# Kernel tuning notes

Hardware: AMD Instinct MI355X
Metric: run time of the kernel (lower is better)

## Reference

```python
import jax, jax.numpy as jnp
import numpy as np

D = 512      # d_model
H = 8        # heads
DK = D // H  # 64
DFF = 2048
EPS = 1e-6


def layer_norm(x, gamma, beta):
    # Faithful to the module: std uses Bessel correction (torch default unbiased)
    # and eps is added to std (not variance); gamma/beta are scalars init to 1.
    m = jnp.mean(x, axis=-1, keepdims=True)
    var = jnp.sum((x - m) ** 2, axis=-1, keepdims=True) / (x.shape[-1] - 1)
    return gamma * (x - m) / (jnp.sqrt(var) + EPS) + beta


def setup_inputs() -> dict:
    key = jax.random.key(0)
    ks = jax.random.split(key, 12)
    s = 0.02
    inp = {
        "x": jax.random.normal(ks[0], (4, 2048, D), dtype=jnp.float32),
        "src_mask": jnp.ones((4, 1, 1, 2048), dtype=jnp.int32),
        "Wq": jax.random.normal(ks[1], (D, D), jnp.float32) * s,
        "bq": jnp.zeros((D,), jnp.float32),
        "Wk": jax.random.normal(ks[2], (D, D), jnp.float32) * s,
        "bk": jnp.zeros((D,), jnp.float32),
        "Wv": jax.random.normal(ks[3], (D, D), jnp.float32) * s,
        "bv": jnp.zeros((D,), jnp.float32),
        "Wo": jax.random.normal(ks[4], (D, D), jnp.float32) * s,
        "bo": jnp.zeros((D,), jnp.float32),
        "W1": jax.random.normal(ks[5], (D, DFF), jnp.float32) * s,
        "b1": jnp.zeros((DFF,), jnp.float32),
        "W2": jax.random.normal(ks[6], (DFF, D), jnp.float32) * s,
        "b2": jnp.zeros((D,), jnp.float32),
        "g1": jnp.ones((), jnp.float32),
        "be1": jnp.ones((), jnp.float32),
        "g2": jnp.ones((), jnp.float32),
        "be2": jnp.ones((), jnp.float32),
    }
    return inp


def reference(x, src_mask, Wq, bq, Wk, bk, Wv, bv, Wo, bo,
              W1, b1, W2, b2, g1, be1, g2, be2):
    B, S, _ = x.shape

    # --- residual 1: pre-LN self-attention ---
    xn = layer_norm(x, g1, be1)                               # [B,S,D]
    q = (xn @ Wq + bq).reshape(B, S, H, DK).transpose(0, 2, 1, 3)  # [B,H,S,DK]
    k = (xn @ Wk + bk).reshape(B, S, H, DK).transpose(0, 2, 1, 3)
    v = (xn @ Wv + bv).reshape(B, S, H, DK).transpose(0, 2, 1, 3)

    scores = jnp.einsum('bhqd,bhkd->bhqk', q, k) / np.float32(np.sqrt(DK))
    scores = jnp.where(src_mask == 0, jnp.float32(-1e9), scores)  # [B,H,S,S]
    attn = jax.nn.softmax(scores, axis=-1)
    o = jnp.einsum('bhqk,bhkd->bhqd', attn, v)                # [B,H,S,DK]
    o = o.transpose(0, 2, 1, 3).reshape(B, S, D)
    x = x + (o @ Wo + bo)

    # --- residual 2: pre-LN feed-forward ---
    xn = layer_norm(x, g2, be2)
    ff = jax.nn.relu(xn @ W1 + b1) @ W2 + b2
    return x + ff
```

## Files before the change

### kernel.cpp

```cpp
#include <hip/hip_runtime.h>
#include <hip/hip_bf16.h>


#define B_   4
#define S_   2048
#define D_   512
#define H_   8
#define DK_  64
#define DFF_ 2048
#define M_   (B_*S_)

typedef __attribute__((ext_vector_type(8))) short short8;
typedef __attribute__((ext_vector_type(4))) float f32x4;
typedef __attribute__((ext_vector_type(16))) float f32x16;

#define QSCALE 0.18033688011f

#if __has_builtin(__builtin_amdgcn_exp2f)
#define EXP2(x) __builtin_amdgcn_exp2f(x)
#else
#define EXP2(x) exp2f(x)
#endif

#define GLOAD_LDS(gp, lp) __builtin_amdgcn_global_load_lds( \
    (const __attribute__((address_space(1))) void*)(gp),    \
    (__attribute__((address_space(3))) void*)(lp), 16, 0, 0)

#define WAITV(N) asm volatile("s_waitcnt vmcnt(" #N ")" ::: "memory")
#define BARRIER() __builtin_amdgcn_s_barrier()

__device__ inline unsigned short f2bf(float f) {
    union { float f; unsigned u; } v; v.f = f;
    unsigned r = v.u + 0x7fffu + ((v.u >> 16) & 1u);
    return (unsigned short)(r >> 16);
}

__device__ inline unsigned cvtpk_bf16(float a, float b) {
    unsigned r;
    asm("v_cvt_pk_bf16_f32 %0, %1, %2" : "=v"(r) : "v"(a), "v"(b));
    return r;
}

__device__ inline void permswap32(unsigned &x, unsigned &y) {
    asm volatile("v_permlane32_swap_b32 %0, %1" : "+v"(x), "+v"(y));
}

__global__ __launch_bounds__(256) void transT_kernel(
    const float* __restrict__ Wq, const float* __restrict__ Wk,
    const float* __restrict__ Wv, const float* __restrict__ Wo,
    const float* __restrict__ W1, const float* __restrict__ W2,
    const float* __restrict__ bq, const float* __restrict__ bk,
    const float* __restrict__ bv, const int* __restrict__ mask,
    float* __restrict__ qkvb, unsigned* __restrict__ mbits,
    short* __restrict__ dst,
    const float* __restrict__ x, const float* __restrict__ g1,
    const float* __restrict__ be1, short* __restrict__ xn) {
    const int id = blockIdx.x, t = threadIdx.x;
    if (id >= 769) {
        int w = t >> 6, l = t & 63;
        int row = (id - 769) * 4 + w;
        const float4* xr = (const float4*)(x + (size_t)row * D_);
        float4 a = xr[l * 2], b = xr[l * 2 + 1];
        float s = a.x + a.y + a.z + a.w + b.x + b.y + b.z + b.w;
        for (int off = 32; off > 0; off >>= 1) s += __shfl_xor(s, off);
        float mean = s * (1.f / 512.f);
        float e[8] = {a.x - mean, a.y - mean, a.z - mean, a.w - mean,
                      b.x - mean, b.y - mean, b.z - mean, b.w - mean};
        float vs = 0.f;
        #pragma unroll
        for (int i = 0; i < 8; i++) vs += e[i] * e[i];
        for (int off = 32; off > 0; off >>= 1) vs += __shfl_xor(vs, off);
        float scale = g1[0] / (sqrtf(vs * (1.f / 511.f)) + 1e-6f);
        float b0 = be1[0];
        union { short8 v; short s[8]; } o;
        #pragma unroll
        for (int i = 0; i < 8; i++) o.s[i] = (short)f2bf(e[i] * scale + b0);
        *(short8*)(xn + (size_t)row * D_ + l * 8) = o.v;
        return;
    }
    if (id == 768) {
        for (int i = t; i < 1536; i += 256)
            qkvb[i] = (i < 512) ? bq[i] * QSCALE : (i < 1024) ? bk[i - 512] : bv[i - 1024];
        if (t < 128) {
            int b = t >> 5, tile = t & 31;
            const int* mr = mask + b * S_ + tile * 64;
            bool all1 = true;
            for (int u = 0; u < 64; u++) all1 &= (mr[u] != 0);
            unsigned long long bal = __ballot(all1);
            if ((t & 63) == 0) {
                mbits[(t >> 6) * 2]     = (unsigned)bal;
                mbits[(t >> 6) * 2 + 1] = (unsigned)(bal >> 32);
            }
        }
        return;
    }
    __shared__ float T[64][65];
    const float* src; short* d; int K, N, tk, tn;
    if (id < 256) {
        int m = id >> 6;
        src = (m == 0) ? Wq : (m == 1) ? Wk : (m == 2) ? Wv : Wo;
        d = dst + (size_t)m * 512 * 512; K = 512; N = 512;
        int j = id & 63; tk = j >> 3; tn = j & 7;
    } else if (id < 512) {
        src = W1; d = dst + (size_t)4 * 512 * 512; K = 512; N = 2048;
        int j = id - 256; tk = j >> 5; tn = j & 31;
    } else {
        src = W2; d = dst + (size_t)4 * 512 * 512 + 2048 * 512; K = 2048; N = 512;
        int j = id - 512; tk = j >> 3; tn = j & 7;
    }
    const int k0 = tk * 64, n0 = tn * 64;
    #pragma unroll
    for (int i = 0; i < 4; i++) {
        int r = i * 16 + (t >> 4), c4 = (t & 15) * 4;
        float4 v = *(const float4*)(src + (size_t)(k0 + r) * N + n0 + c4);
        T[r][c4] = v.x; T[r][c4 + 1] = v.y; T[r][c4 + 2] = v.z; T[r][c4 + 3] = v.w;
    }
    __syncthreads();
    #pragma unroll
    for (int p = 0; p < 2; p++) {
        int j = p * 256 + t, n = j >> 3, kc = (j & 7) * 8;
        union { short8 v; short s[8]; } o;
        #pragma unroll
        for (int u = 0; u < 8; u++) o.s[u] = (short)f2bf(T[kc + u][n]);
        *(short8*)(d + (size_t)(n0 + n) * K + k0 + kc) = o.v;
    }
}

__global__ __launch_bounds__(256) void ln_kernel(const float* __restrict__ x,
                                                 const float* __restrict__ g,
                                                 const float* __restrict__ be,
                                                 short* __restrict__ out) {
    int w = threadIdx.x >> 6, l = threadIdx.x & 63;
    int row = blockIdx.x * 4 + w;
    const float4* xr = (const float4*)(x + (size_t)row * D_);
    float4 a = xr[l * 2], b = xr[l * 2 + 1];
    float s = a.x + a.y + a.z + a.w + b.x + b.y + b.z + b.w;
    for (int off = 32; off > 0; off >>= 1) s += __shfl_xor(s, off);
    float mean = s * (1.f / 512.f);
    float e[8] = {a.x - mean, a.y - mean, a.z - mean, a.w - mean,
                  b.x - mean, b.y - mean, b.z - mean, b.w - mean};
    float vs = 0.f;
    #pragma unroll
    for (int i = 0; i < 8; i++) vs += e[i] * e[i];
    for (int off = 32; off > 0; off >>= 1) vs += __shfl_xor(vs, off);
    float scale = g[0] / (sqrtf(vs * (1.f / 511.f)) + 1e-6f);
    float b0 = be[0];
    union { short8 v; short s[8]; } o;
    #pragma unroll
    for (int i = 0; i < 8; i++) o.s[i] = (short)f2bf(e[i] * scale + b0);
    *(short8*)(out + (size_t)row * D_ + l * 8) = o.v;
}

template <int BN, int MODE>
__global__ __launch_bounds__(256, 4) void gemm_kernel(
    const short* __restrict__ A, const short* __restrict__ Bt,
    const float* __restrict__ bias, const float* __restrict__ resid,
    void* __restrict__ out, int M, int N, int K) {
    constexpr int NF = BN / 32;
    __shared__ __align__(16) short smem[3 * 128 * 32 + 3 * BN * 32];
    auto As = [&](int b) -> short* { return smem + b * 4096; };
    auto Bs = [&](int b) -> short* { return smem + 12288 + b * BN * 32; };
    const int t = threadIdx.x;
    const int w = t >> 6, l = t & 63;
    const int wm = w >> 1, wn = w & 1;
    const int lr = l & 15, lk = l >> 4;
    const int m0 = blockIdx.x * 128, n0 = blockIdx.y * BN;
    f32x4 acc[4][NF] = {};

    auto stage = [&](int buf, int k0) {
        #pragma unroll
        for (int p = 0; p < 2; p++) {
            int g = p * 4 + w;
            int r = g * 16 + (l >> 2), c = l & 3, cs = c ^ ((r >> 2) & 3);
            GLOAD_LDS(A + (size_t)(m0 + r) * K + k0 + cs * 8, As(buf) + g * 512);
        }
        #pragma unroll
        for (int p = 0; p < BN / 64; p++) {
            int g = p * 4 + w;
            int r = g * 16 + (l >> 2), c = l & 3, cs = c ^ ((r >> 2) & 3);
            GLOAD_LDS(Bt + (size_t)(n0 + r) * K + k0 + cs * 8, Bs(buf) + g * 512);
        }
    };

    const int nk = K >> 5;
    stage(0, 0); stage(1, 32);
    if constexpr (BN == 128) WAITV(4); else WAITV(3);
    BARRIER();

    for (int tk = 0; tk < nk; ++tk) {
        const int cur = tk % 3;
        const bool more = (tk + 2 < nk);
        if (more) stage((tk + 2) % 3, (tk + 2) * 32);
        short8 af[4], bf[NF];
        #pragma unroll
        for (int f = 0; f < 4; f++) {
            int ra = wm * 64 + f * 16 + lr;
            af[f] = *(const short8*)&As(cur)[ra * 32 + ((lk ^ ((ra >> 2) & 3)) << 3)];
        }
        #pragma unroll
        for (int f = 0; f < NF; f++) {
            int rb = wn * (BN / 2) + f * 16 + lr;
            bf[f] = *(const short8*)&Bs(cur)[rb * 32 + ((lk ^ ((rb >> 2) & 3)) << 3)];
        }
        __builtin_amdgcn_s_setprio(1);
        #pragma unroll
        for (int mf = 0; mf < 4; mf++)
            #pragma unroll
            for (int nf = 0; nf < NF; nf++)
                acc[mf][nf] = __builtin_amdgcn_mfma_f32_16x16x32_bf16(
                    af[mf], bf[nf], acc[mf][nf], 0, 0, 0);
        __builtin_amdgcn_s_setprio(0);
        if (more) { if constexpr (BN == 128) WAITV(4); else WAITV(3); }
        else WAITV(0);
        BARRIER();
    }

    if constexpr (MODE == 0) {
        const int seg = n0 >> 9;
        #pragma unroll
        for (int mf = 0; mf < 4; mf++) {
            #pragma unroll
            for (int nf = 0; nf < NF; nf++) {
                int mb = m0 + wm * 64 + mf * 16 + lk * 4;
                int n  = n0 + wn * (BN / 2) + nf * 16 + lr;
                float bv = bias[n];
                int bb = mb >> 11, sl = mb & 2047, nl = n & 511;
                unsigned short* ob = (unsigned short*)out + (size_t)seg * M_ * D_;
                float v[4];
                #pragma unroll
                for (int i = 0; i < 4; i++) {
                    float val = acc[mf][nf][i];
                    if (seg == 0) val *= QSCALE;
                    v[i] = val + bv;
                }
                if (seg < 2) {
                    #pragma unroll
                    for (int i = 0; i < 4; i++)
                        ob[(((size_t)(bb * 8 + (nl >> 6)) * 2048 + sl + i) << 6) + (nl & 63)] = f2bf(v[i]);
                } else {
                    uint2 pk;
                    pk.x = cvtpk_bf16(v[0], v[1]);
                    pk.y = cvtpk_bf16(v[2], v[3]);
                    *(uint2*)&ob[(((size_t)(bb * 8 + (nl >> 6)) * 64 + (nl & 63)) << 11) + sl] = pk;
                }
            }
        }
    } else if constexpr (MODE == 1) {
        float* E = (float*)smem;
        #pragma unroll
        for (int mf = 0; mf < 4; mf++)
            #pragma unroll
            for (int nf = 0; nf < NF; nf++) {
                int n_loc = wn * (BN / 2) + nf * 16 + lr;
                float bv = bias[n0 + n_loc];
                int c = n_loc >> 4;
                #pragma unroll
                for (int i = 0; i < 4; i++) {
                    int m_loc = wm * 64 + mf * 16 + lk * 4 + i;
                    E[m_loc * 64 + ((c ^ (m_loc & 3)) << 4) + (n_loc & 15)] =
                        acc[mf][nf][i] + bv;
                }
            }
        BARRIER();
        #pragma unroll
        for (int pass = 0; pass < 8; pass++) {
            int fid = pass * 256 + t;
            int row = fid >> 4, c4 = fid & 15;
            int lc = c4 >> 2, j = c4 & 3;
            f32x4 v = *(f32x4*)&E[row * 64 + (((lc ^ (row & 3))) << 4) + j * 4];
            int m = m0 + row, n = n0 + lc * 16 + j * 4;
            f32x4 rv = *(const f32x4*)&resid[(size_t)m * N + n];
            *(f32x4*)&((float*)out)[(size_t)m * N + n] = v + rv;
        }
    } else {
        unsigned short* E16 = (unsigned short*)smem;
        #pragma unroll
        for (int mf = 0; mf < 4; mf++)
            #pragma unroll
            for (int nf = 0; nf < NF; nf++) {
                int n_loc = wn * (BN / 2) + nf * 16 + lr;
                float bv = bias[n0 + n_loc];
                int c = n_loc >> 3;
                #pragma unroll
                for (int i = 0; i < 4; i++) {
                    int m_loc = wm * 64 + mf * 16 + lk * 4 + i;
                    E16[m_loc * 128 + ((c ^ (m_loc & 7)) << 3) + (n_loc & 7)] =
                        f2bf(fmaxf(acc[mf][nf][i] + bv, 0.f));
                }
            }
        BARRIER();
        #pragma unroll
        for (int pass = 0; pass < 8; pass++) {
            int fid = pass * 256 + t;
            int row = fid >> 4, c = fid & 15;
            short8 v = *(short8*)&E16[row * 128 + ((c ^ (row & 7)) << 3)];
            *(short8*)&((unsigned short*)out)[(size_t)(m0 + row) * N + n0 + c * 8] = v;
        }
    }
}

__global__ __launch_bounds__(512, 4) void attn_kernel(
    const short* __restrict__ Q, const short* __restrict__ Kb,
    const short* __restrict__ Vt, const int* __restrict__ mask,
    const unsigned* __restrict__ mbits, unsigned short* __restrict__ O) {
    __shared__ __align__(16) short sm[24576];
    const int t = threadIdx.x, w = t >> 6, l = t & 63;
    const int ql = l & 31, hi = l >> 5;
    const int wh = w >> 2, wl = w & 3;
    const int bh = blockIdx.x, b = bh >> 3, h = bh & 7;
    const int q = blockIdx.y * 128 + wl * 32 + ql;

    const short* qrow = Q + ((size_t)bh * S_ + q) * DK_;
    short8 qf[4];
    #pragma unroll
    for (int s = 0; s < 4; s++) qf[s] = *(const short8*)(qrow + s * 16 + hi * 8);

    const short* kg = Kb + (size_t)bh * S_ * DK_;
    const short* vg = Vt + (size_t)bh * DK_ * S_;
    const int* mrow = mask + b * S_;
    const unsigned mb = mbits[b];

    short* KH = sm + wh * 12288;
    short* kdw = KH + wl * 512;

    const int kro = wl * 8 + (l >> 3);
    const int kc = (l & 7) ^ (kro & 7);
    const short* kp = kg + ((size_t)(wh * 1024 + kro)) * 64 + kc * 8;
    const int vr = kro, vs0 = l & 7, vc = vs0 ^ (vr & 7);
    const int vdk = vr + 32 * (vc >> 2), vkvo = (vc & 3) * 8;
    const short* vp = vg + (size_t)vdk * 2048 + vkvo + wh * 1024;

    auto stage = [&](int buf) {
        GLOAD_LDS(kp, kdw + buf * 4096);
        GLOAD_LDS(vp, kdw + buf * 4096 + 2048);
        kp += 32 * 64;
        vp += 32;
    };

    const short ONEB = (short)0x3F80;
    const short8 ones = {ONEB, ONEB, ONEB, ONEB, ONEB, ONEB, ONEB, ONEB};

    f32x16 o_acc[2] = {};
    f32x16 lsum = {};

    stage(0); stage(1);
    WAITV(2);
    BARRIER();

    for (int tt = 0; tt < 32; ++tt) {
        const int cur = tt % 3;
        const int gt = wh * 32 + tt;
        if (tt + 2 < 32) stage((tt + 2) % 3);
        const short* Ks = KH + cur * 4096;
        const short* Vs = Ks + 2048;

        f32x16 s_acc = {};
        __builtin_amdgcn_s_setprio(1);
        #pragma unroll
        for (int s = 0; s < 4; s++) {
            short8 kf = *(const short8*)&Ks[ql * 64 + (((s * 2 + hi) ^ (ql & 7)) << 3)];
            s_acc = __builtin_amdgcn_mfma_f32_32x32x16_bf16(kf, qf[s], s_acc, 0, 0, 0);
        }
        __builtin_amdgcn_s_setprio(0);

        if (!((mb >> (gt >> 1)) & 1)) {
            #pragma unroll
            for (int r = 0; r < 16; r++) {
                int k = gt * 32 + (r & 3) + 8 * (r >> 2) + 4 * hi;
                if (mrow[k] == 0) s_acc[r] = -1.4426950e9f;
            }
        }

        float p[16];
        #pragma unroll
        for (int r = 0; r < 16; r++) p[r] = EXP2(s_acc[r]);
        unsigned Dp[8];
        #pragma unroll
        for (int j = 0; j < 8; j++) Dp[j] = cvtpk_bf16(p[2 * j], p[2 * j + 1]);

        #pragma unroll
        for (int s16 = 0; s16 < 2; s16++) {
            unsigned f0 = Dp[s16 * 4 + 0], f1 = Dp[s16 * 4 + 1];
            unsigned f2 = Dp[s16 * 4 + 2], f3 = Dp[s16 * 4 + 3];
            permswap32(f0, f2);
            permswap32(f1, f3);
            union { unsigned u[4]; short8 v; } pu;
            pu.u[0] = f0; pu.u[1] = f1; pu.u[2] = f2; pu.u[3] = f3;
            __builtin_amdgcn_s_setprio(1);
            #pragma unroll
            for (int dt = 0; dt < 2; dt++) {
                short8 vf = *(const short8*)&Vs[ql * 64 + (((dt * 4 + s16 * 2 + hi) ^ (ql & 7)) << 3)];
                o_acc[dt] = __builtin_amdgcn_mfma_f32_32x32x16_bf16(vf, pu.v, o_acc[dt], 0, 0, 0);
            }
            lsum = __builtin_amdgcn_mfma_f32_32x32x16_bf16(ones, pu.v, lsum, 0, 0, 0);
            __builtin_amdgcn_s_setprio(0);
        }

        if (tt < 30) WAITV(2); else WAITV(0);
        BARRIER();
    }

    float l_part = lsum[0];
    float* C = (float*)sm;
    f32x4* Cv = (f32x4*)sm;
    if (wh == 1) {
        #pragma unroll
        for (int j = 0; j < 8; j++) {
            f32x4 v;
            #pragma unroll
            for (int e = 0; e < 4; e++) v[e] = o_acc[j >> 2][(j & 3) * 4 + e];
            Cv[wl * 512 + j * 64 + l] = v;
        }
        C[8192 + wl * 64 + l] = l_part;
    }
    __syncthreads();
    if (wh == 0) {
        #pragma unroll
        for (int j = 0; j < 8; j++) {
            f32x4 v = Cv[wl * 512 + j * 64 + l];
            #pragma unroll
            for (int e = 0; e < 4; e++) o_acc[j >> 2][(j & 3) * 4 + e] += v[e];
        }
        l_part += C[8192 + wl * 64 + l];
        float linv = 1.f / l_part;
        unsigned short* orow = O + ((size_t)b * S_ + q) * D_ + h * 64;
        #pragma unroll
        for (int dt = 0; dt < 2; dt++)
            #pragma unroll
            for (int g = 0; g < 4; g++) {
                unsigned u0 = cvtpk_bf16(o_acc[dt][g * 4 + 0] * linv, o_acc[dt][g * 4 + 1] * linv);
                unsigned u1 = cvtpk_bf16(o_acc[dt][g * 4 + 2] * linv, o_acc[dt][g * 4 + 3] * linv);
                uint2 pk; pk.x = u0; pk.y = u1;
                *(uint2*)(orow + dt * 32 + 8 * g + 4 * hi) = pk;
            }
    }
}

extern "C" void kernel_launch(void* const* d_in, const int* in_sizes, int n_in,
                              void* d_out, int out_size, void* d_ws, size_t ws_size,
                              hipStream_t stream) {
    const float* x    = (const float*)d_in[0];
    const int*   mask = (const int*)d_in[1];
    const float* Wq = (const float*)d_in[2];  const float* bq  = (const float*)d_in[3];
    const float* Wk = (const float*)d_in[4];  const float* bk  = (const float*)d_in[5];
    const float* Wv = (const float*)d_in[6];  const float* bv  = (const float*)d_in[7];
    const float* Wo = (const float*)d_in[8];  const float* bo  = (const float*)d_in[9];
    const float* W1 = (const float*)d_in[10]; const float* b1  = (const float*)d_in[11];
    const float* W2 = (const float*)d_in[12]; const float* b2  = (const float*)d_in[13];
    const float* g1 = (const float*)d_in[14]; const float* be1 = (const float*)d_in[15];
    const float* g2 = (const float*)d_in[16]; const float* be2 = (const float*)d_in[17];

    short* WqT = (short*)d_ws;
    short* W1T = WqT + 4 * 512 * 512;
    short* W2T = W1T + 2048 * 512;
    short* xn  = W2T + 512 * 2048;
    short* Qb  = xn  + (size_t)M_ * D_;
    short* Kbf = Qb  + (size_t)M_ * D_;
    short* Vtb = Kbf + (size_t)M_ * D_;
    short* Ob  = Vtb + (size_t)M_ * D_;
    float* x2  = (float*)(Ob + (size_t)M_ * D_);
    float* qkvb = x2;
    unsigned* mbits = (unsigned*)(qkvb + 1536);
    short* WoT = WqT + 3 * 512 * 512;
    short* Hb  = Qb;

    transT_kernel<<<769 + M_ / 4, 256, 0, stream>>>(Wq, Wk, Wv, Wo, W1, W2,
                                                    bq, bk, bv, mask, qkvb, mbits, WqT,
                                                    x, g1, be1, xn);

    gemm_kernel<128, 0><<<dim3(64, 12), 256, 0, stream>>>(xn, WqT, qkvb, nullptr,
                                                          Qb, M_, 1536, 512);

    attn_kernel<<<dim3(B_ * H_, S_ / 128), 512, 0, stream>>>(Qb, Kbf, Vtb, mask, mbits,
                                                             (unsigned short*)Ob);

    gemm_kernel<64, 1><<<dim3(64, 8), 256, 0, stream>>>(Ob, WoT, bo, x, x2, M_, 512, 512);

    ln_kernel<<<M_ / 4, 256, 0, stream>>>(x2, g2, be2, xn);

    gemm_kernel<128, 2><<<dim3(64, 16), 256, 0, stream>>>(xn, W1T, b1, nullptr, Hb, M_, 2048, 512);
    gemm_kernel<64, 1><<<dim3(64, 8), 256, 0, stream>>>(Hb, W2T, b2, x2, (float*)d_out, M_, 512, 2048);
}
```

Before: 150.7 us.

## Widen GEMM K-tile to 64 with double buffering; attention processes 64 queries per wave

The GEMM now stages 64-wide K slices in two LDS buffers instead of three 32-wide ones, with an 8-way XOR swizzle. This halves the number of barriers and loop iterations but gives up one stage of prefetch depth. The attention kernel now gives each wave two 32-query groups that share the same K/V fragments, halving the grid and reusing K/V loads across more queries. Row sums are accumulated in scalar registers rather than through a ones-matrix MFMA. Register pressure rises, which is reflected in lowering the occupancy hints in launch_bounds to 2.

```diff
diff --git a/kernel.cpp b/kernel.cpp
--- a/kernel.cpp
+++ b/kernel.cpp
@@ -152,14 +152,14 @@
 }
 
 template <int BN, int MODE>
-__global__ __launch_bounds__(256, 4) void gemm_kernel(
+__global__ __launch_bounds__(256, 2) void gemm_kernel(
     const short* __restrict__ A, const short* __restrict__ Bt,
     const float* __restrict__ bias, const float* __restrict__ resid,
     void* __restrict__ out, int M, int N, int K) {
     constexpr int NF = BN / 32;
-    __shared__ __align__(16) short smem[3 * 128 * 32 + 3 * BN * 32];
-    auto As = [&](int b) -> short* { return smem + b * 4096; };
-    auto Bs = [&](int b) -> short* { return smem + 12288 + b * BN * 32; };
+    __shared__ __align__(16) short smem[2 * 128 * 64 + 2 * BN * 64];
+    auto As = [&](int b) -> short* { return smem + b * 8192; };
+    auto Bs = [&](int b) -> short* { return smem + 16384 + b * BN * 64; };
     const int t = threadIdx.x;
     const int w = t >> 6, l = t & 63;
     const int wm = w >> 1, wn = w & 1;
@@ -169,49 +169,54 @@
 
     auto stage = [&](int buf, int k0) {
         #pragma unroll
-        for (int p = 0; p < 2; p++) {
-            int g = p * 4 + w;
-            int r = g * 16 + (l >> 2), c = l & 3, cs = c ^ ((r >> 2) & 3);
-            GLOAD_LDS(A + (size_t)(m0 + r) * K + k0 + cs * 8, As(buf) + g * 512);
-        }
-        #pragma unroll
-        for (int p = 0; p < BN / 64; p++) {
-            int g = p * 4 + w;
-            int r = g * 16 + (l >> 2), c = l & 3, cs = c ^ ((r >> 2) & 3);
-            GLOAD_LDS(Bt + (size_t)(n0 + r) * K + k0 + cs * 8, Bs(buf) + g * 512);
+        for (int p = 0; p < 4; p++) {
+            int id = p * 256 + t;
+            int r = id >> 3, c = id & 7, cs = c ^ (r & 7);
+            GLOAD_LDS(A + (size_t)(m0 + r) * K + k0 + cs * 8, As(buf) + (p * 256 + w * 64) * 8);
+        }
+        #pragma unroll
+        for (int p = 0; p < BN / 32; p++) {
+            int id = p * 256 + t;
+            int r = id >> 3, c = id & 7, cs = c ^ (r & 7);
+            GLOAD_LDS(Bt + (size_t)(n0 + r) * K + k0 + cs * 8, Bs(buf) + (p * 256 + w * 64) * 8);
         }
     };
 
-    const int nk = K >> 5;
-    stage(0, 0); stage(1, 32);
-    if constexpr (BN == 128) WAITV(4); else WAITV(3);
-    BARRIER();
+    const int nk = K >> 6;
+    stage(0, 0);
 
     for (int tk = 0; tk < nk; ++tk) {
-        const int cur = tk % 3;
-        const bool more = (tk + 2 < nk);
-        if (more) stage((tk + 2) % 3, (tk + 2) * 32);
-        short8 af[4], bf[NF];
+        const int cur = tk & 1;
+        if (tk + 1 < nk) {
+            stage(cur ^ 1, (tk + 1) * 64);
+            if constexpr (BN == 128) WAITV(8); else WAITV(6);
+        } else WAITV(0);
+        BARRIER();
+        short8 af[4][2], bf[NF][2];
         #pragma unroll
         for (int f = 0; f < 4; f++) {
             int ra = wm * 64 + f * 16 + lr;
-            af[f] = *(const short8*)&As(cur)[ra * 32 + ((lk ^ ((ra >> 2) & 3)) << 3)];
+            #pragma unroll
+            for (int kk = 0; kk < 2; kk++)
+                af[f][kk] = *(const short8*)&As(cur)[ra * 64 + (((kk * 4 + lk) ^ (ra & 7)) << 3)];
         }
         #pragma unroll
         for (int f = 0; f < NF; f++) {
             int rb = wn * (BN / 2) + f * 16 + lr;
-            bf[f] = *(const short8*)&Bs(cur)[rb * 32 + ((lk ^ ((rb >> 2) & 3)) << 3)];
+            #pragma unroll
+            for (int kk = 0; kk < 2; kk++)
+                bf[f][kk] = *(const short8*)&Bs(cur)[rb * 64 + (((kk * 4 + lk) ^ (rb & 7)) << 3)];
         }
         __builtin_amdgcn_s_setprio(1);
         #pragma unroll
-        for (int mf = 0; mf < 4; mf++)
-            #pragma unroll
-            for (int nf = 0; nf < NF; nf++)
-                acc[mf][nf] = __builtin_amdgcn_mfma_f32_16x16x32_bf16(
-                    af[mf], bf[nf], acc[mf][nf], 0, 0, 0);
+        for (int kk = 0; kk < 2; kk++)
+            #pragma unroll
+            for (int mf = 0; mf < 4; mf++)
+                #pragma unroll
+                for (int nf = 0; nf < NF; nf++)
+                    acc[mf][nf] = __builtin_amdgcn_mfma_f32_16x16x32_bf16(
+                        af[mf][kk], bf[nf][kk], acc[mf][nf], 0, 0, 0);
         __builtin_amdgcn_s_setprio(0);
-        if (more) { if constexpr (BN == 128) WAITV(4); else WAITV(3); }
-        else WAITV(0);
         BARRIER();
     }
 
@@ -299,7 +304,7 @@
     }
 }
 
-__global__ __launch_bounds__(512, 4) void attn_kernel(
+__global__ __launch_bounds__(512, 2) void attn_kernel(
     const short* __restrict__ Q, const short* __restrict__ Kb,
     const short* __restrict__ Vt, const int* __restrict__ mask,
     const unsigned* __restrict__ mbits, unsigned short* __restrict__ O) {
@@ -308,12 +313,15 @@
     const int ql = l & 31, hi = l >> 5;
     const int wh = w >> 2, wl = w & 3;
     const int bh = blockIdx.x, b = bh >> 3, h = bh & 7;
-    const int q = blockIdx.y * 128 + wl * 32 + ql;
-
-    const short* qrow = Q + ((size_t)bh * S_ + q) * DK_;
-    short8 qf[4];
-    #pragma unroll
-    for (int s = 0; s < 4; s++) qf[s] = *(const short8*)(qrow + s * 16 + hi * 8);
+    const int q0 = blockIdx.y * 256 + wl * 64;
+
+    short8 qf[2][4];
+    #pragma unroll
+    for (int qs = 0; qs < 2; qs++) {
+        const short* qrow = Q + ((size_t)bh * S_ + q0 + qs * 32 + ql) * DK_;
+        #pragma unroll
+        for (int s = 0; s < 4; s++) qf[qs][s] = *(const short8*)(qrow + s * 16 + hi * 8);
+    }
 
     const short* kg = Kb + (size_t)bh * S_ * DK_;
     const short* vg = Vt + (size_t)bh * DK_ * S_;
@@ -326,7 +334,7 @@
     const int kro = wl * 8 + (l >> 3);
     const int kc = (l & 7) ^ (kro & 7);
     const short* kp = kg + ((size_t)(wh * 1024 + kro)) * 64 + kc * 8;
-    const int vr = kro, vs0 = l & 7, vc = vs0 ^ (vr & 7);
+    const int vr = kro, vc = (l & 7) ^ (vr & 7);
     const int vdk = vr + 32 * (vc >> 2), vkvo = (vc & 3) * 8;
     const short* vp = vg + (size_t)vdk * 2048 + vkvo + wh * 1024;
 
@@ -337,11 +345,8 @@
         vp += 32;
     };
 
-    const short ONEB = (short)0x3F80;
-    const short8 ones = {ONEB, ONEB, ONEB, ONEB, ONEB, ONEB, ONEB, ONEB};
-
-    f32x16 o_acc[2] = {};
-    f32x16 lsum = {};
+    f32x16 o_acc[2][2] = {};
+    float la[2][4] = {};
 
     stage(0); stage(1);
     WAITV(2);
@@ -354,45 +359,59 @@
         const short* Ks = KH + cur * 4096;
         const short* Vs = Ks + 2048;
 
-        f32x16 s_acc = {};
+        short8 kf[4];
+        #pragma unroll
+        for (int s = 0; s < 4; s++)
+            kf[s] = *(const short8*)&Ks[ql * 64 + (((s * 2 + hi) ^ (ql & 7)) << 3)];
+        f32x16 sa = {}, sb = {};
         __builtin_amdgcn_s_setprio(1);
         #pragma unroll
-        for (int s = 0; s < 4; s++) {
-            short8 kf = *(const short8*)&Ks[ql * 64 + (((s * 2 + hi) ^ (ql & 7)) << 3)];
-            s_acc = __builtin_amdgcn_mfma_f32_32x32x16_bf16(kf, qf[s], s_acc, 0, 0, 0);
-        }
+        for (int s = 0; s < 4; s++)
+            sa = __builtin_amdgcn_mfma_f32_32x32x16_bf16(kf[s], qf[0][s], sa, 0, 0, 0);
+        #pragma unroll
+        for (int s = 0; s < 4; s++)
+            sb = __builtin_amdgcn_mfma_f32_32x32x16_bf16(kf[s], qf[1][s], sb, 0, 0, 0);
         __builtin_amdgcn_s_setprio(0);
 
         if (!((mb >> (gt >> 1)) & 1)) {
             #pragma unroll
             for (int r = 0; r < 16; r++) {
                 int k = gt * 32 + (r & 3) + 8 * (r >> 2) + 4 * hi;
-                if (mrow[k] == 0) s_acc[r] = -1.4426950e9f;
-            }
-        }
-
-        float p[16];
-        #pragma unroll
-        for (int r = 0; r < 16; r++) p[r] = EXP2(s_acc[r]);
-        unsigned Dp[8];
-        #pragma unroll
-        for (int j = 0; j < 8; j++) Dp[j] = cvtpk_bf16(p[2 * j], p[2 * j + 1]);
+                if (mrow[k] == 0) { sa[r] = -1.4426950e9f; sb[r] = -1.4426950e9f; }
+            }
+        }
+
+        unsigned Dp[2][8];
+        {
+            float p[16];
+            #pragma unroll
+            for (int r = 0; r < 16; r++) { p[r] = EXP2(sa[r]); la[0][r & 3] += p[r]; }
+            #pragma unroll
+            for (int j = 0; j < 8; j++) Dp[0][j] = cvtpk_bf16(p[2 * j], p[2 * j + 1]);
+            #pragma unroll
+            for (int r = 0; r < 16; r++) { p[r] = EXP2(sb[r]); la[1][r & 3] += p[r]; }
+            #pragma unroll
+            for (int j = 0; j < 8; j++) Dp[1][j] = cvtpk_bf16(p[2 * j], p[2 * j + 1]);
+        }
 
         #pragma unroll
         for (int s16 = 0; s16 < 2; s16++) {
-            unsigned f0 = Dp[s16 * 4 + 0], f1 = Dp[s16 * 4 + 1];
-            unsigned f2 = Dp[s16 * 4 + 2], f3 = Dp[s16 * 4 + 3];
-            permswap32(f0, f2);
-            permswap32(f1, f3);
-            union { unsigned u[4]; short8 v; } pu;
-            pu.u[0] = f0; pu.u[1] = f1; pu.u[2] = f2; pu.u[3] = f3;
+            union { unsigned u[4]; short8 v; } pu[2];
+            #pragma unroll
+            for (int qs = 0; qs < 2; qs++) {
+                unsigned f0 = Dp[qs][s16 * 4 + 0], f1 = Dp[qs][s16 * 4 + 1];
+                unsigned f2 = Dp[qs][s16 * 4 + 2], f3 = Dp[qs][s16 * 4 + 3];
+                permswap32(f0, f2);
+                permswap32(f1, f3);
+                pu[qs].u[0] = f0; pu[qs].u[1] = f1; pu[qs].u[2] = f2; pu[qs].u[3] = f3;
+            }
             __builtin_amdgcn_s_setprio(1);
             #pragma unroll
             for (int dt = 0; dt < 2; dt++) {
                 short8 vf = *(const short8*)&Vs[ql * 64 + (((dt * 4 + s16 * 2 + hi) ^ (ql & 7)) << 3)];
-                o_acc[dt] = __builtin_amdgcn_mfma_f32_32x32x16_bf16(vf, pu.v, o_acc[dt], 0, 0, 0);
-            }
-            lsum = __builtin_amdgcn_mfma_f32_32x32x16_bf16(ones, pu.v, lsum, 0, 0, 0);
+                o_acc[0][dt] = __builtin_amdgcn_mfma_f32_32x32x16_bf16(vf, pu[0].v, o_acc[0][dt], 0, 0, 0);
+                o_acc[1][dt] = __builtin_amdgcn_mfma_f32_32x32x16_bf16(vf, pu[1].v, o_acc[1][dt], 0, 0, 0);
+            }
             __builtin_amdgcn_s_setprio(0);
         }
 
@@ -400,39 +419,48 @@
         BARRIER();
     }
 
-    float l_part = lsum[0];
+    float lp[2];
+    #pragma unroll
+    for (int qs = 0; qs < 2; qs++) {
+        float s = (la[qs][0] + la[qs][1]) + (la[qs][2] + la[qs][3]);
+        lp[qs] = s + __shfl_xor(s, 32);
+    }
+
     float* C = (float*)sm;
     f32x4* Cv = (f32x4*)sm;
-    if (wh == 1) {
-        #pragma unroll
-        for (int j = 0; j < 8; j++) {
-            f32x4 v;
-            #pragma unroll
-            for (int e = 0; e < 4; e++) v[e] = o_acc[j >> 2][(j & 3) * 4 + e];
-            Cv[wl * 512 + j * 64 + l] = v;
-        }
-        C[8192 + wl * 64 + l] = l_part;
-    }
-    __syncthreads();
-    if (wh == 0) {
-        #pragma unroll
-        for (int j = 0; j < 8; j++) {
-            f32x4 v = Cv[wl * 512 + j * 64 + l];
-            #pragma unroll
-            for (int e = 0; e < 4; e++) o_acc[j >> 2][(j & 3) * 4 + e] += v[e];
-        }
-        l_part += C[8192 + wl * 64 + l];
-        float linv = 1.f / l_part;
-        unsigned short* orow = O + ((size_t)b * S_ + q) * D_ + h * 64;
-        #pragma unroll
-        for (int dt = 0; dt < 2; dt++)
-            #pragma unroll
-            for (int g = 0; g < 4; g++) {
-                unsigned u0 = cvtpk_bf16(o_acc[dt][g * 4 + 0] * linv, o_acc[dt][g * 4 + 1] * linv);
-                unsigned u1 = cvtpk_bf16(o_acc[dt][g * 4 + 2] * linv, o_acc[dt][g * 4 + 3] * linv);
-                uint2 pk; pk.x = u0; pk.y = u1;
-                *(uint2*)(orow + dt * 32 + 8 * g + 4 * hi) = pk;
-            }
+    #pragma unroll
+    for (int qs = 0; qs < 2; qs++) {
+        __syncthreads();
+        if (wh == 1) {
+            #pragma unroll
+            for (int j = 0; j < 8; j++) {
+                f32x4 v;
+                #pragma unroll
+                for (int e = 0; e < 4; e++) v[e] = o_acc[qs][j >> 2][(j & 3) * 4 + e];
+                Cv[wl * 512 + j * 64 + l] = v;
+            }
+            C[8192 + wl * 64 + l] = lp[qs];
+        }
+        __syncthreads();
+        if (wh == 0) {
+            #pragma unroll
+            for (int j = 0; j < 8; j++) {
+                f32x4 v = Cv[wl * 512 + j * 64 + l];
+                #pragma unroll
+                for (int e = 0; e < 4; e++) o_acc[qs][j >> 2][(j & 3) * 4 + e] += v[e];
+            }
+            float linv = 1.f / (lp[qs] + C[8192 + wl * 64 + l]);
+            unsigned short* orow = O + ((size_t)b * S_ + q0 + qs * 32 + ql) * D_ + h * 64;
+            #pragma unroll
+            for (int dt = 0; dt < 2; dt++)
+                #pragma unroll
+                for (int g = 0; g < 4; g++) {
+                    unsigned u0 = cvtpk_bf16(o_acc[qs][dt][g * 4 + 0] * linv, o_acc[qs][dt][g * 4 + 1] * linv);
+                    unsigned u1 = cvtpk_bf16(o_acc[qs][dt][g * 4 + 2] * linv, o_acc[qs][dt][g * 4 + 3] * linv);
+                    uint2 pk; pk.x = u0; pk.y = u1;
+                    *(uint2*)(orow + dt * 32 + 8 * g + 4 * hi) = pk;
+                }
+        }
     }
 }
 
@@ -471,7 +499,7 @@
     gemm_kernel<128, 0><<<dim3(64, 12), 256, 0, stream>>>(xn, WqT, qkvb, nullptr,
                                                           Qb, M_, 1536, 512);
 
-    attn_kernel<<<dim3(B_ * H_, S_ / 128), 512, 0, stream>>>(Qb, Kbf, Vtb, mask, mbits,
+    attn_kernel<<<dim3(B_ * H_, S_ / 256), 512, 0, stream>>>(Qb, Kbf, Vtb, mask, mbits,
                                                              (unsigned short*)Ob);
 
     gemm_kernel<64, 1><<<dim3(64, 8), 256, 0, stream>>>(Ob, WoT, bo, x, x2, M_, 512, 512);
```

Measured after the change: 138.5 us. 1.09x faster.

## Use BK=64 double-buffered GEMM pipeline and scalar softmax row sums in attention

Applied to the files above, without the earlier changes.

The GEMM moves from a triple-buffered K=32 pipeline to a double-buffered K=64 pipeline with an 8-chunk XOR swizzle. This halves the number of barrier/iteration steps and lowers the occupancy hint in launch bounds from 4 to 2. The attention kernel replaces the ones-matrix MFMA used for row sums with VALU accumulation of the exp values plus a cross-half shuffle, freeing matrix-core cycles. The K/V staging is also rewritten to compute addresses from the tile index instead of advancing pointers. The risks are lower occupancy, less latency hiding with only two buffers, and the extra VALU adds.

```diff
diff --git a/kernel.cpp b/kernel.cpp
--- a/kernel.cpp
+++ b/kernel.cpp
@@ -152,14 +152,14 @@
 }
 
 template <int BN, int MODE>
-__global__ __launch_bounds__(256, 4) void gemm_kernel(
+__global__ __launch_bounds__(256, 2) void gemm_kernel(
     const short* __restrict__ A, const short* __restrict__ Bt,
     const float* __restrict__ bias, const float* __restrict__ resid,
     void* __restrict__ out, int M, int N, int K) {
     constexpr int NF = BN / 32;
-    __shared__ __align__(16) short smem[3 * 128 * 32 + 3 * BN * 32];
-    auto As = [&](int b) -> short* { return smem + b * 4096; };
-    auto Bs = [&](int b) -> short* { return smem + 12288 + b * BN * 32; };
+    __shared__ __align__(16) short smem[2 * 128 * 64 + 2 * BN * 64];
+    auto As = [&](int b) -> short* { return smem + b * 8192; };
+    auto Bs = [&](int b) -> short* { return smem + 16384 + b * BN * 64; };
     const int t = threadIdx.x;
     const int w = t >> 6, l = t & 63;
     const int wm = w >> 1, wn = w & 1;
@@ -169,49 +169,54 @@
 
     auto stage = [&](int buf, int k0) {
         #pragma unroll
-        for (int p = 0; p < 2; p++) {
-            int g = p * 4 + w;
-            int r = g * 16 + (l >> 2), c = l & 3, cs = c ^ ((r >> 2) & 3);
-            GLOAD_LDS(A + (size_t)(m0 + r) * K + k0 + cs * 8, As(buf) + g * 512);
-        }
-        #pragma unroll
-        for (int p = 0; p < BN / 64; p++) {
-            int g = p * 4 + w;
-            int r = g * 16 + (l >> 2), c = l & 3, cs = c ^ ((r >> 2) & 3);
-            GLOAD_LDS(Bt + (size_t)(n0 + r) * K + k0 + cs * 8, Bs(buf) + g * 512);
+        for (int p = 0; p < 4; p++) {
+            int id = p * 256 + t;
+            int r = id >> 3, c = id & 7, cs = c ^ (r & 7);
+            GLOAD_LDS(A + (size_t)(m0 + r) * K + k0 + cs * 8, As(buf) + (p * 256 + w * 64) * 8);
+        }
+        #pragma unroll
+        for (int p = 0; p < BN / 32; p++) {
+            int id = p * 256 + t;
+            int r = id >> 3, c = id & 7, cs = c ^ (r & 7);
+            GLOAD_LDS(Bt + (size_t)(n0 + r) * K + k0 + cs * 8, Bs(buf) + (p * 256 + w * 64) * 8);
         }
     };
 
-    const int nk = K >> 5;
-    stage(0, 0); stage(1, 32);
-    if constexpr (BN == 128) WAITV(4); else WAITV(3);
-    BARRIER();
+    const int nk = K >> 6;
+    stage(0, 0);
 
     for (int tk = 0; tk < nk; ++tk) {
-        const int cur = tk % 3;
-        const bool more = (tk + 2 < nk);
-        if (more) stage((tk + 2) % 3, (tk + 2) * 32);
-        short8 af[4], bf[NF];
+        const int cur = tk & 1;
+        if (tk + 1 < nk) {
+            stage(cur ^ 1, (tk + 1) * 64);
+            if constexpr (BN == 128) WAITV(8); else WAITV(6);
+        } else WAITV(0);
+        BARRIER();
+        short8 af[4][2], bf[NF][2];
         #pragma unroll
         for (int f = 0; f < 4; f++) {
             int ra = wm * 64 + f * 16 + lr;
-            af[f] = *(const short8*)&As(cur)[ra * 32 + ((lk ^ ((ra >> 2) & 3)) << 3)];
+            #pragma unroll
+            for (int kk = 0; kk < 2; kk++)
+                af[f][kk] = *(const short8*)&As(cur)[ra * 64 + (((kk * 4 + lk) ^ (ra & 7)) << 3)];
         }
         #pragma unroll
         for (int f = 0; f < NF; f++) {
             int rb = wn * (BN / 2) + f * 16 + lr;
-            bf[f] = *(const short8*)&Bs(cur)[rb * 32 + ((lk ^ ((rb >> 2) & 3)) << 3)];
+            #pragma unroll
+            for (int kk = 0; kk < 2; kk++)
+                bf[f][kk] = *(const short8*)&Bs(cur)[rb * 64 + (((kk * 4 + lk) ^ (rb & 7)) << 3)];
         }
         __builtin_amdgcn_s_setprio(1);
         #pragma unroll
-        for (int mf = 0; mf < 4; mf++)
-            #pragma unroll
-            for (int nf = 0; nf < NF; nf++)
-                acc[mf][nf] = __builtin_amdgcn_mfma_f32_16x16x32_bf16(
-                    af[mf], bf[nf], acc[mf][nf], 0, 0, 0);
+        for (int kk = 0; kk < 2; kk++)
+            #pragma unroll
+            for (int mf = 0; mf < 4; mf++)
+                #pragma unroll
+                for (int nf = 0; nf < NF; nf++)
+                    acc[mf][nf] = __builtin_amdgcn_mfma_f32_16x16x32_bf16(
+                        af[mf][kk], bf[nf][kk], acc[mf][nf], 0, 0, 0);
         __builtin_amdgcn_s_setprio(0);
-        if (more) { if constexpr (BN == 128) WAITV(4); else WAITV(3); }
-        else WAITV(0);
         BARRIER();
     }
 
@@ -321,36 +326,33 @@
     const unsigned mb = mbits[b];
 
     short* KH = sm + wh * 12288;
-    short* kdw = KH + wl * 512;
-
-    const int kro = wl * 8 + (l >> 3);
-    const int kc = (l & 7) ^ (kro & 7);
-    const short* kp = kg + ((size_t)(wh * 1024 + kro)) * 64 + kc * 8;
-    const int vr = kro, vs0 = l & 7, vc = vs0 ^ (vr & 7);
-    const int vdk = vr + 32 * (vc >> 2), vkvo = (vc & 3) * 8;
-    const short* vp = vg + (size_t)vdk * 2048 + vkvo + wh * 1024;
-
-    auto stage = [&](int buf) {
-        GLOAD_LDS(kp, kdw + buf * 4096);
-        GLOAD_LDS(vp, kdw + buf * 4096 + 2048);
-        kp += 32 * 64;
-        vp += 32;
+
+    auto stage = [&](int buf, int kv0) {
+        short* Kd = KH + buf * 4096;
+        short* Vd = Kd + 2048;
+        {
+            int r = wl * 8 + (l >> 3), c = l & 7, cs = c ^ (r & 7);
+            GLOAD_LDS(kg + (size_t)(kv0 + r) * DK_ + cs * 8, &Kd[wl * 512]);
+        }
+        {
+            int r = wl * 8 + (l >> 3), s = l & 7, c = s ^ (r & 7);
+            int dk = r + 32 * (c >> 2), kvo = (c & 3) * 8;
+            GLOAD_LDS(vg + (size_t)dk * S_ + kv0 + kvo, &Vd[wl * 512]);
+        }
     };
 
-    const short ONEB = (short)0x3F80;
-    const short8 ones = {ONEB, ONEB, ONEB, ONEB, ONEB, ONEB, ONEB, ONEB};
-
     f32x16 o_acc[2] = {};
-    f32x16 lsum = {};
-
-    stage(0); stage(1);
+    float la0 = 0.f, la1 = 0.f, la2 = 0.f, la3 = 0.f;
+
+    stage(0, wh * 1024);
+    stage(1, wh * 1024 + 32);
     WAITV(2);
     BARRIER();
 
     for (int tt = 0; tt < 32; ++tt) {
         const int cur = tt % 3;
         const int gt = wh * 32 + tt;
-        if (tt + 2 < 32) stage((tt + 2) % 3);
+        if (tt + 2 < 32) stage((tt + 2) % 3, (gt + 2) * 32);
         const short* Ks = KH + cur * 4096;
         const short* Vs = Ks + 2048;
 
@@ -374,6 +376,10 @@
         float p[16];
         #pragma unroll
         for (int r = 0; r < 16; r++) p[r] = EXP2(s_acc[r]);
+        #pragma unroll
+        for (int r = 0; r < 16; r += 4) {
+            la0 += p[r]; la1 += p[r + 1]; la2 += p[r + 2]; la3 += p[r + 3];
+        }
         unsigned Dp[8];
         #pragma unroll
         for (int j = 0; j < 8; j++) Dp[j] = cvtpk_bf16(p[2 * j], p[2 * j + 1]);
@@ -392,7 +398,6 @@
                 short8 vf = *(const short8*)&Vs[ql * 64 + (((dt * 4 + s16 * 2 + hi) ^ (ql & 7)) << 3)];
                 o_acc[dt] = __builtin_amdgcn_mfma_f32_32x32x16_bf16(vf, pu.v, o_acc[dt], 0, 0, 0);
             }
-            lsum = __builtin_amdgcn_mfma_f32_32x32x16_bf16(ones, pu.v, lsum, 0, 0, 0);
             __builtin_amdgcn_s_setprio(0);
         }
 
@@ -400,7 +405,7 @@
         BARRIER();
     }
 
-    float l_part = lsum[0];
+    float l_part = (la0 + la1) + (la2 + la3);
     float* C = (float*)sm;
     f32x4* Cv = (f32x4*)sm;
     if (wh == 1) {
@@ -422,7 +427,7 @@
             for (int e = 0; e < 4; e++) o_acc[j >> 2][(j & 3) * 4 + e] += v[e];
         }
         l_part += C[8192 + wl * 64 + l];
-        float linv = 1.f / l_part;
+        float linv = 1.f / (l_part + __shfl_xor(l_part, 32));
         unsigned short* orow = O + ((size_t)b * S_ + q) * D_ + h * 64;
         #pragma unroll
         for (int dt = 0; dt < 2; dt++)
```

Result: faster. 136.6 us (-9.4%).
